# Kernel tuning notes

Measured on AMD Instinct MI355X. Metric: run time of the kernel, lower is better.

## Reference

```python
import jax, jax.numpy as jnp
import numpy as np
import math

D_MODEL = 1024
HEAD_DIM = 64
B, T = 4, 4096


def setup_inputs() -> dict:
    key = jax.random.key(0)
    kx, kq, kk, kv = jax.random.split(key, 4)
    s = 1.0 / math.sqrt(D_MODEL)  # torch Linear default init scale (approx, uniform->normal ok for ref)
    return {
        "x": jax.random.normal(kx, (B, T, D_MODEL), dtype=jnp.float32),
        "Wq": jax.random.normal(kq, (HEAD_DIM, D_MODEL), dtype=jnp.float32) * s,
        "Wk": jax.random.normal(kk, (HEAD_DIM, D_MODEL), dtype=jnp.float32) * s,
        "Wv": jax.random.normal(kv, (HEAD_DIM, D_MODEL), dtype=jnp.float32) * s,
        "energy": jnp.asarray(1.0, dtype=jnp.float32),
    }


def reference(x, Wq, Wk, Wv, energy):
    # Projections: nn.Linear(d_model, head_dim, bias=False) -> x @ W.T
    q = jnp.einsum("btc,hc->bth", x, Wq)  # [B,T,H]
    k = jnp.einsum("btc,hc->bth", x, Wk)
    v = jnp.einsum("btc,hc->bth", x, Wv)

    scale = 1.0 / math.sqrt(HEAD_DIM)
    scores = jnp.einsum("bqh,bkh->bqk", q, k) * scale  # [B,T,T]
    attn = jax.nn.softmax(scores, axis=-1)
    out = jnp.einsum("bqk,bkh->bqh", attn, v)  # [B,T,H]

    # Entropy of attention rows, averaged over batch and queries
    attn_entropy = -jnp.sum(attn * jnp.log(attn + 1e-8), axis=-1).mean()
    # Metabolic EMA side-effect (stateful in torch; returned here for completeness)
    new_energy = 0.9 * energy + 0.1 * attn_entropy

    return out, attn, new_energy
```

## Files before the change

### kernel.cpp

```cpp
#include <hip/hip_runtime.h>

#define PITCH 72

typedef __attribute__((ext_vector_type(8))) short bf16x8;
typedef __attribute__((ext_vector_type(4))) float f32x4;
typedef __attribute__((ext_vector_type(8))) unsigned short u16x8;

__device__ __forceinline__ unsigned short f2bf(float f) {
  union { float f; unsigned int u; } v; v.f = f;
  unsigned int u = v.u + 0x7fffu + ((v.u >> 16) & 1u);
  return (unsigned short)(u >> 16);
}

__device__ __forceinline__ f32x4 mfma16(bf16x8 a, bf16x8 b, f32x4 c) {
  return __builtin_amdgcn_mfma_f32_16x16x32_bf16(a, b, c, 0, 0, 0);
}

__global__ __launch_bounds__(256) void qkv_kernel(
    const float* __restrict__ x, const float* __restrict__ Wq,
    const float* __restrict__ Wk, const float* __restrict__ Wv,
    unsigned short* __restrict__ q_ws, unsigned short* __restrict__ k_ws,
    unsigned short* __restrict__ vT_ws) {
  __shared__ unsigned short Xs[64 * PITCH];
  __shared__ unsigned short Ws[192 * PITCH];

  const int tid = threadIdx.x;
  const int wave = tid >> 6, lane = tid & 63;
  const int quad = lane >> 4, l16 = lane & 15;
  const int m0 = blockIdx.x * 64;

  f32x4 acc[12];
#pragma unroll
  for (int i = 0; i < 12; ++i) acc[i] = (f32x4)0.0f;

  for (int k0 = 0; k0 < 1024; k0 += 64) {
#pragma unroll
    for (int i = 0; i < 4; ++i) {
      int cc = tid + i * 256;
      int row = cc >> 4, c4 = cc & 15;
      float4 f = *(const float4*)(x + (size_t)(m0 + row) * 1024 + k0 + c4 * 4);
      unsigned short h0 = f2bf(f.x), h1 = f2bf(f.y), h2 = f2bf(f.z), h3 = f2bf(f.w);
      ushort4 h = make_ushort4(h0, h1, h2, h3);
      *(ushort4*)&Xs[row * PITCH + c4 * 4] = h;
    }
#pragma unroll
    for (int i = 0; i < 12; ++i) {
      int cc = tid + i * 256;
      int row = cc >> 4, c4 = cc & 15;
      int which = row >> 6, wrow = row & 63;
      const float* wp = (which == 0) ? Wq : ((which == 1) ? Wk : Wv);
      float4 f = *(const float4*)(wp + (size_t)wrow * 1024 + k0 + c4 * 4);
      ushort4 h = make_ushort4(f2bf(f.x), f2bf(f.y), f2bf(f.z), f2bf(f.w));
      *(ushort4*)&Ws[row * PITCH + c4 * 4] = h;
    }
    __syncthreads();
#pragma unroll
    for (int ks = 0; ks < 64; ks += 32) {
      bf16x8 a = *(const bf16x8*)&Xs[(wave * 16 + l16) * PITCH + ks + quad * 8];
#pragma unroll
      for (int nt = 0; nt < 12; ++nt) {
        bf16x8 b = *(const bf16x8*)&Ws[(nt * 16 + l16) * PITCH + ks + quad * 8];
        acc[nt] = mfma16(a, b, acc[nt]);
      }
    }
    __syncthreads();
  }

  const int mrow = wave * 16 + quad * 4;
#pragma unroll
  for (int nt = 0; nt < 4; ++nt)
#pragma unroll
    for (int r = 0; r < 4; ++r) {
      int m = m0 + mrow + r;
      int h = nt * 16 + l16;
      q_ws[(size_t)m * 64 + h] = f2bf(acc[nt][r] * 0.125f);
    }
#pragma unroll
  for (int nt = 0; nt < 4; ++nt)
#pragma unroll
    for (int r = 0; r < 4; ++r) {
      int m = m0 + mrow + r;
      int h = nt * 16 + l16;
      k_ws[(size_t)m * 64 + h] = f2bf(acc[nt + 4][r]);
    }
  __syncthreads();
#pragma unroll
  for (int nt = 0; nt < 4; ++nt)
#pragma unroll
    for (int r = 0; r < 4; ++r)
      Xs[(nt * 16 + l16) * PITCH + mrow + r] = f2bf(acc[nt + 8][r]);
  __syncthreads();
  const int b = m0 >> 12, t0 = m0 & 4095;
#pragma unroll
  for (int i = 0; i < 2; ++i) {
    int cc = tid + i * 256;
    int h = cc >> 3, c8 = cc & 7;
    u16x8 v = *(const u16x8*)&Xs[h * PITCH + c8 * 8];
    *(u16x8*)(vT_ws + ((size_t)b * 64 + h) * 4096 + t0 + c8 * 8) = v;
  }
}

__global__ __launch_bounds__(256) void attn_kernel(
    const unsigned short* __restrict__ q_ws, const unsigned short* __restrict__ k_ws,
    const unsigned short* __restrict__ vT_ws, float* __restrict__ out,
    float* __restrict__ attn, float* __restrict__ entAcc) {
  __shared__ unsigned short Qs[64 * PITCH];
  __shared__ unsigned short Ks[64 * PITCH];
  __shared__ unsigned short Vts[64 * PITCH];
  __shared__ unsigned short Ps[4][16 * PITCH];
  __shared__ float rowS[64], rowW[64], invS[64];

  const int tid = threadIdx.x;
  const int wave = tid >> 6, lane = tid & 63;
  const int quad = lane >> 4, l16 = lane & 15;
  const int bx = blockIdx.x;
  const int b = bx >> 6, q0 = (bx & 63) * 64;

  const unsigned short* qb = q_ws + ((size_t)b * 4096 + q0) * 64;
  const unsigned short* kb = k_ws + (size_t)b * 4096 * 64;
  const unsigned short* vtb = vT_ws + (size_t)b * 64 * 4096;

#pragma unroll
  for (int i = 0; i < 2; ++i) {
    int cc = tid + i * 256;
    int row = cc >> 3, c8 = cc & 7;
    *(u16x8*)&Qs[row * PITCH + c8 * 8] = *(const u16x8*)(qb + (size_t)row * 64 + c8 * 8);
  }

  f32x4 Oacc[4];
#pragma unroll
  for (int i = 0; i < 4; ++i) Oacc[i] = (f32x4)0.0f;
  float sumE[4] = {0.f, 0.f, 0.f, 0.f};
  float sumES[4] = {0.f, 0.f, 0.f, 0.f};

  __syncthreads();

  for (int kt = 0; kt < 64; ++kt) {
    const int k0 = kt * 64;
#pragma unroll
    for (int i = 0; i < 2; ++i) {
      int cc = tid + i * 256;
      int row = cc >> 3, c8 = cc & 7;
      *(u16x8*)&Ks[row * PITCH + c8 * 8] =
          *(const u16x8*)(kb + (size_t)(k0 + row) * 64 + c8 * 8);
      *(u16x8*)&Vts[row * PITCH + c8 * 8] =
          *(const u16x8*)(vtb + (size_t)row * 4096 + k0 + c8 * 8);
    }
    __syncthreads();

    f32x4 s[4];
#pragma unroll
    for (int i = 0; i < 4; ++i) s[i] = (f32x4)0.0f;
#pragma unroll
    for (int ks = 0; ks < 64; ks += 32) {
      bf16x8 a = *(const bf16x8*)&Qs[(wave * 16 + l16) * PITCH + ks + quad * 8];
#pragma unroll
      for (int nt = 0; nt < 4; ++nt) {
        bf16x8 bk = *(const bf16x8*)&Ks[(nt * 16 + l16) * PITCH + ks + quad * 8];
        s[nt] = mfma16(a, bk, s[nt]);
      }
    }
#pragma unroll
    for (int nt = 0; nt < 4; ++nt)
#pragma unroll
      for (int r = 0; r < 4; ++r) {
        float sv = s[nt][r];
        float e = __expf(sv);
        sumE[r] += e;
        sumES[r] += e * sv;
        Ps[wave][(quad * 4 + r) * PITCH + nt * 16 + l16] = f2bf(e);
      }
#pragma unroll
    for (int kk = 0; kk < 64; kk += 32) {
      bf16x8 a = *(const bf16x8*)&Ps[wave][l16 * PITCH + kk + quad * 8];
#pragma unroll
      for (int ht = 0; ht < 4; ++ht) {
        bf16x8 bv = *(const bf16x8*)&Vts[(ht * 16 + l16) * PITCH + kk + quad * 8];
        Oacc[ht] = mfma16(a, bv, Oacc[ht]);
      }
    }
    __syncthreads();
  }

#pragma unroll
  for (int off = 1; off < 16; off <<= 1)
#pragma unroll
    for (int r = 0; r < 4; ++r) {
      sumE[r] += __shfl_xor(sumE[r], off, 64);
      sumES[r] += __shfl_xor(sumES[r], off, 64);
    }
  if (l16 == 0)
#pragma unroll
    for (int r = 0; r < 4; ++r) {
      rowS[wave * 16 + quad * 4 + r] = sumE[r];
      rowW[wave * 16 + quad * 4 + r] = sumES[r];
    }
  __syncthreads();
  if (tid < 64) {
    float S = rowS[tid], W = rowW[tid];
    float inv = 1.0f / S;
    invS[tid] = inv;
    float ent = __logf(S) - W * inv;
#pragma unroll
    for (int off = 1; off < 64; off <<= 1) ent += __shfl_xor(ent, off, 64);
    if (tid == 0) atomicAdd(entAcc, ent);
  }
  __syncthreads();

  float invR[4];
#pragma unroll
  for (int r = 0; r < 4; ++r) invR[r] = invS[wave * 16 + quad * 4 + r];

#pragma unroll
  for (int ht = 0; ht < 4; ++ht)
#pragma unroll
    for (int r = 0; r < 4; ++r) {
      int m = q0 + wave * 16 + quad * 4 + r;
      out[((size_t)b * 4096 + m) * 64 + ht * 16 + l16] = Oacc[ht][r] * invR[r];
    }

  float* attnb = attn + (size_t)b * 4096 * 4096;
  for (int kt = 0; kt < 64; ++kt) {
    const int k0 = kt * 64;
    __syncthreads();
#pragma unroll
    for (int i = 0; i < 2; ++i) {
      int cc = tid + i * 256;
      int row = cc >> 3, c8 = cc & 7;
      *(u16x8*)&Ks[row * PITCH + c8 * 8] =
          *(const u16x8*)(kb + (size_t)(k0 + row) * 64 + c8 * 8);
    }
    __syncthreads();

    f32x4 s[4];
#pragma unroll
    for (int i = 0; i < 4; ++i) s[i] = (f32x4)0.0f;
#pragma unroll
    for (int ks = 0; ks < 64; ks += 32) {
      bf16x8 a = *(const bf16x8*)&Qs[(wave * 16 + l16) * PITCH + ks + quad * 8];
#pragma unroll
      for (int nt = 0; nt < 4; ++nt) {
        bf16x8 bk = *(const bf16x8*)&Ks[(nt * 16 + l16) * PITCH + ks + quad * 8];
        s[nt] = mfma16(a, bk, s[nt]);
      }
    }
#pragma unroll
    for (int nt = 0; nt < 4; ++nt)
#pragma unroll
      for (int r = 0; r < 4; ++r) {
        float p = __expf(s[nt][r]) * invR[r];
        attnb[(size_t)(q0 + wave * 16 + quad * 4 + r) * 4096 + k0 + nt * 16 + l16] = p;
      }
  }
}

__global__ void energy_kernel(const float* __restrict__ energy,
                              const float* __restrict__ entAcc,
                              float* __restrict__ dst) {
  if (threadIdx.x == 0 && blockIdx.x == 0)
    dst[0] = 0.9f * energy[0] + 0.1f * (entAcc[0] * (1.0f / 16384.0f));
}

extern "C" void kernel_launch(void* const* d_in, const int* in_sizes, int n_in,
                              void* d_out, int out_size, void* d_ws, size_t ws_size,
                              hipStream_t stream) {
  (void)in_sizes; (void)n_in; (void)out_size; (void)ws_size;
  const float* x = (const float*)d_in[0];
  const float* Wq = (const float*)d_in[1];
  const float* Wk = (const float*)d_in[2];
  const float* Wv = (const float*)d_in[3];
  const float* energy = (const float*)d_in[4];

  float* out = (float*)d_out;
  float* attn = out + (size_t)4 * 4096 * 64;
  float* dst_energy = attn + (size_t)4 * 4096 * 4096;

  char* ws = (char*)d_ws;
  float* entAcc = (float*)ws;
  unsigned short* q_ws = (unsigned short*)(ws + 256);
  unsigned short* k_ws = q_ws + (size_t)16384 * 64;
  unsigned short* vT_ws = k_ws + (size_t)16384 * 64;

  hipMemsetAsync(entAcc, 0, sizeof(float), stream);
  qkv_kernel<<<256, 256, 0, stream>>>(x, Wq, Wk, Wv, q_ws, k_ws, vT_ws);
  attn_kernel<<<256, 256, 0, stream>>>(q_ws, k_ws, vT_ws, out, attn, entAcc);
  energy_kernel<<<1, 64, 0, stream>>>(energy, entAcc, dst_energy);
}
```

Measured before the change: 528.6 us.

## Split attention into split-K flash pass, combine, and parallel attn-matrix writer

The QKV projection now runs one block per (row tile, projection), giving 768 blocks instead of 256. The fused attention kernel is split into three kernels. A flash pass splits the key range four ways and writes partial outputs and row sums. A combine kernel reduces those partials, normalizes the output and computes entropy. A separate 8192-block kernel recomputes the scores and writes the normalized attention matrix. The aim is to fix low occupancy, since the old design had only 256 blocks each looping over all keys twice, and to spread the large attn store across many blocks. In exchange it adds workspace round-trips for the partials and extra kernel launches, and the QKV split reloads x three times.

```diff
diff --git a/kernel.cpp b/kernel.cpp
--- a/kernel.cpp
+++ b/kernel.cpp
@@ -1,6 +1,7 @@
 #include <hip/hip_runtime.h>
 
 #define PITCH 72
+#define PPITCH 68
 
 typedef __attribute__((ext_vector_type(8))) short bf16x8;
 typedef __attribute__((ext_vector_type(4))) float f32x4;
@@ -22,99 +23,91 @@
     unsigned short* __restrict__ q_ws, unsigned short* __restrict__ k_ws,
     unsigned short* __restrict__ vT_ws) {
   __shared__ unsigned short Xs[64 * PITCH];
-  __shared__ unsigned short Ws[192 * PITCH];
-
-  const int tid = threadIdx.x;
-  const int wave = tid >> 6, lane = tid & 63;
-  const int quad = lane >> 4, l16 = lane & 15;
-  const int m0 = blockIdx.x * 64;
-
-  f32x4 acc[12];
-#pragma unroll
-  for (int i = 0; i < 12; ++i) acc[i] = (f32x4)0.0f;
-
-  for (int k0 = 0; k0 < 1024; k0 += 64) {
-#pragma unroll
-    for (int i = 0; i < 4; ++i) {
-      int cc = tid + i * 256;
-      int row = cc >> 4, c4 = cc & 15;
-      float4 f = *(const float4*)(x + (size_t)(m0 + row) * 1024 + k0 + c4 * 4);
-      unsigned short h0 = f2bf(f.x), h1 = f2bf(f.y), h2 = f2bf(f.z), h3 = f2bf(f.w);
-      ushort4 h = make_ushort4(h0, h1, h2, h3);
-      *(ushort4*)&Xs[row * PITCH + c4 * 4] = h;
-    }
-#pragma unroll
-    for (int i = 0; i < 12; ++i) {
-      int cc = tid + i * 256;
-      int row = cc >> 4, c4 = cc & 15;
-      int which = row >> 6, wrow = row & 63;
-      const float* wp = (which == 0) ? Wq : ((which == 1) ? Wk : Wv);
-      float4 f = *(const float4*)(wp + (size_t)wrow * 1024 + k0 + c4 * 4);
-      ushort4 h = make_ushort4(f2bf(f.x), f2bf(f.y), f2bf(f.z), f2bf(f.w));
-      *(ushort4*)&Ws[row * PITCH + c4 * 4] = h;
-    }
-    __syncthreads();
-#pragma unroll
-    for (int ks = 0; ks < 64; ks += 32) {
-      bf16x8 a = *(const bf16x8*)&Xs[(wave * 16 + l16) * PITCH + ks + quad * 8];
-#pragma unroll
-      for (int nt = 0; nt < 12; ++nt) {
-        bf16x8 b = *(const bf16x8*)&Ws[(nt * 16 + l16) * PITCH + ks + quad * 8];
-        acc[nt] = mfma16(a, b, acc[nt]);
-      }
-    }
-    __syncthreads();
-  }
-
-  const int mrow = wave * 16 + quad * 4;
-#pragma unroll
-  for (int nt = 0; nt < 4; ++nt)
-#pragma unroll
-    for (int r = 0; r < 4; ++r) {
-      int m = m0 + mrow + r;
-      int h = nt * 16 + l16;
-      q_ws[(size_t)m * 64 + h] = f2bf(acc[nt][r] * 0.125f);
-    }
-#pragma unroll
-  for (int nt = 0; nt < 4; ++nt)
-#pragma unroll
-    for (int r = 0; r < 4; ++r) {
-      int m = m0 + mrow + r;
-      int h = nt * 16 + l16;
-      k_ws[(size_t)m * 64 + h] = f2bf(acc[nt + 4][r]);
-    }
-  __syncthreads();
-#pragma unroll
-  for (int nt = 0; nt < 4; ++nt)
-#pragma unroll
-    for (int r = 0; r < 4; ++r)
-      Xs[(nt * 16 + l16) * PITCH + mrow + r] = f2bf(acc[nt + 8][r]);
-  __syncthreads();
-  const int b = m0 >> 12, t0 = m0 & 4095;
-#pragma unroll
-  for (int i = 0; i < 2; ++i) {
-    int cc = tid + i * 256;
-    int h = cc >> 3, c8 = cc & 7;
-    u16x8 v = *(const u16x8*)&Xs[h * PITCH + c8 * 8];
-    *(u16x8*)(vT_ws + ((size_t)b * 64 + h) * 4096 + t0 + c8 * 8) = v;
-  }
-}
-
-__global__ __launch_bounds__(256) void attn_kernel(
-    const unsigned short* __restrict__ q_ws, const unsigned short* __restrict__ k_ws,
-    const unsigned short* __restrict__ vT_ws, float* __restrict__ out,
-    float* __restrict__ attn, float* __restrict__ entAcc) {
-  __shared__ unsigned short Qs[64 * PITCH];
-  __shared__ unsigned short Ks[64 * PITCH];
-  __shared__ unsigned short Vts[64 * PITCH];
-  __shared__ unsigned short Ps[4][16 * PITCH];
-  __shared__ float rowS[64], rowW[64], invS[64];
+  __shared__ unsigned short Ws[64 * PITCH];
 
   const int tid = threadIdx.x;
   const int wave = tid >> 6, lane = tid & 63;
   const int quad = lane >> 4, l16 = lane & 15;
   const int bx = blockIdx.x;
-  const int b = bx >> 6, q0 = (bx & 63) * 64;
+  const int mt = bx / 3, which = bx - mt * 3;
+  const int m0 = mt * 64;
+  const float* wp = (which == 0) ? Wq : ((which == 1) ? Wk : Wv);
+
+  f32x4 acc[4];
+#pragma unroll
+  for (int i = 0; i < 4; ++i) acc[i] = (f32x4)0.0f;
+
+  const int srow = tid >> 4, sc4 = tid & 15;
+  for (int k0 = 0; k0 < 1024; k0 += 64) {
+#pragma unroll
+    for (int i = 0; i < 4; ++i) {
+      int row = srow + i * 16;
+      float4 f = *(const float4*)(x + (size_t)(m0 + row) * 1024 + k0 + sc4 * 4);
+      *(ushort4*)&Xs[row * PITCH + sc4 * 4] =
+          make_ushort4(f2bf(f.x), f2bf(f.y), f2bf(f.z), f2bf(f.w));
+      float4 g = *(const float4*)(wp + (size_t)row * 1024 + k0 + sc4 * 4);
+      *(ushort4*)&Ws[row * PITCH + sc4 * 4] =
+          make_ushort4(f2bf(g.x), f2bf(g.y), f2bf(g.z), f2bf(g.w));
+    }
+    __syncthreads();
+#pragma unroll
+    for (int ks = 0; ks < 64; ks += 32) {
+      bf16x8 a = *(const bf16x8*)&Xs[(wave * 16 + l16) * PITCH + ks + quad * 8];
+#pragma unroll
+      for (int nt = 0; nt < 4; ++nt) {
+        bf16x8 b = *(const bf16x8*)&Ws[(nt * 16 + l16) * PITCH + ks + quad * 8];
+        acc[nt] = mfma16(a, b, acc[nt]);
+      }
+    }
+    __syncthreads();
+  }
+
+  const int mrow = wave * 16 + quad * 4;
+  if (which == 0) {
+#pragma unroll
+    for (int nt = 0; nt < 4; ++nt)
+#pragma unroll
+      for (int r = 0; r < 4; ++r)
+        q_ws[(size_t)(m0 + mrow + r) * 64 + nt * 16 + l16] = f2bf(acc[nt][r] * 0.125f);
+  } else if (which == 1) {
+#pragma unroll
+    for (int nt = 0; nt < 4; ++nt)
+#pragma unroll
+      for (int r = 0; r < 4; ++r)
+        k_ws[(size_t)(m0 + mrow + r) * 64 + nt * 16 + l16] = f2bf(acc[nt][r]);
+  } else {
+#pragma unroll
+    for (int nt = 0; nt < 4; ++nt)
+#pragma unroll
+      for (int r = 0; r < 4; ++r)
+        Xs[(nt * 16 + l16) * PITCH + mrow + r] = f2bf(acc[nt + 0][r]);
+    __syncthreads();
+    const int b = m0 >> 12, t0 = m0 & 4095;
+#pragma unroll
+    for (int i = 0; i < 2; ++i) {
+      int cc = tid + i * 256;
+      int h = cc >> 3, c8 = cc & 7;
+      u16x8 v = *(const u16x8*)&Xs[h * PITCH + c8 * 8];
+      *(u16x8*)(vT_ws + ((size_t)b * 64 + h) * 4096 + t0 + c8 * 8) = v;
+    }
+  }
+}
+
+__global__ __launch_bounds__(256) void flash_kernel(
+    const unsigned short* __restrict__ q_ws, const unsigned short* __restrict__ k_ws,
+    const unsigned short* __restrict__ vT_ws, float* __restrict__ Opart,
+    float* __restrict__ Spart, float* __restrict__ Wpart) {
+  __shared__ unsigned short Qs[64 * PITCH];
+  __shared__ unsigned short Ks[64 * PITCH];
+  __shared__ unsigned short Vts[64 * PITCH];
+  __shared__ unsigned short Ps[4][16 * PPITCH];
+
+  const int tid = threadIdx.x;
+  const int wave = tid >> 6, lane = tid & 63;
+  const int quad = lane >> 4, l16 = lane & 15;
+  const int bx = blockIdx.x;
+  const int ksp = bx & 3, qt = (bx >> 2) & 63, b = bx >> 8;
+  const int q0 = qt * 64;
 
   const unsigned short* qb = q_ws + ((size_t)b * 4096 + q0) * 64;
   const unsigned short* kb = k_ws + (size_t)b * 4096 * 64;
@@ -135,7 +128,7 @@
 
   __syncthreads();
 
-  for (int kt = 0; kt < 64; ++kt) {
+  for (int kt = ksp * 16; kt < ksp * 16 + 16; ++kt) {
     const int k0 = kt * 64;
 #pragma unroll
     for (int i = 0; i < 2; ++i) {
@@ -168,11 +161,11 @@
         float e = __expf(sv);
         sumE[r] += e;
         sumES[r] += e * sv;
-        Ps[wave][(quad * 4 + r) * PITCH + nt * 16 + l16] = f2bf(e);
+        Ps[wave][(quad * 4 + r) * PPITCH + nt * 16 + l16] = f2bf(e);
       }
 #pragma unroll
     for (int kk = 0; kk < 64; kk += 32) {
-      bf16x8 a = *(const bf16x8*)&Ps[wave][l16 * PITCH + kk + quad * 8];
+      bf16x8 a = *(const bf16x8*)&Ps[wave][l16 * PPITCH + kk + quad * 8];
 #pragma unroll
       for (int ht = 0; ht < 4; ++ht) {
         bf16x8 bv = *(const bf16x8*)&Vts[(ht * 16 + l16) * PITCH + kk + quad * 8];
@@ -189,17 +182,39 @@
       sumE[r] += __shfl_xor(sumE[r], off, 64);
       sumES[r] += __shfl_xor(sumES[r], off, 64);
     }
+  const int mrow = wave * 16 + quad * 4;
   if (l16 == 0)
 #pragma unroll
     for (int r = 0; r < 4; ++r) {
-      rowS[wave * 16 + quad * 4 + r] = sumE[r];
-      rowW[wave * 16 + quad * 4 + r] = sumES[r];
-    }
-  __syncthreads();
+      Spart[(size_t)bx * 64 + mrow + r] = sumE[r];
+      Wpart[(size_t)bx * 64 + mrow + r] = sumES[r];
+    }
+  float* Op = Opart + (size_t)bx * 4096;
+#pragma unroll
+  for (int ht = 0; ht < 4; ++ht)
+#pragma unroll
+    for (int r = 0; r < 4; ++r)
+      Op[(size_t)(mrow + r) * 64 + ht * 16 + l16] = Oacc[ht][r];
+}
+
+__global__ __launch_bounds__(256) void combine_kernel(
+    const float* __restrict__ Opart, const float* __restrict__ Spart,
+    const float* __restrict__ Wpart, float* __restrict__ out,
+    float* __restrict__ invS, float* __restrict__ entAcc) {
+  __shared__ float invLds[64];
+  const int tid = threadIdx.x;
+  const int bx = blockIdx.x;
+
   if (tid < 64) {
-    float S = rowS[tid], W = rowW[tid];
+    float S = 0.f, W = 0.f;
+#pragma unroll
+    for (int ks = 0; ks < 4; ++ks) {
+      S += Spart[(size_t)(bx * 4 + ks) * 64 + tid];
+      W += Wpart[(size_t)(bx * 4 + ks) * 64 + tid];
+    }
     float inv = 1.0f / S;
-    invS[tid] = inv;
+    invS[(size_t)bx * 64 + tid] = inv;
+    invLds[tid] = inv;
     float ent = __logf(S) - W * inv;
 #pragma unroll
     for (int off = 1; off < 64; off <<= 1) ent += __shfl_xor(ent, off, 64);
@@ -207,51 +222,77 @@
   }
   __syncthreads();
 
+  const int r = tid >> 2, cg = tid & 3;
+  float inv = invLds[r];
+#pragma unroll
+  for (int j = 0; j < 4; ++j) {
+    int c = cg * 16 + j * 4;
+    f32x4 s = (f32x4)0.0f;
+#pragma unroll
+    for (int ks = 0; ks < 4; ++ks)
+      s += *(const f32x4*)(Opart + (size_t)(bx * 4 + ks) * 4096 + r * 64 + c);
+    s *= inv;
+    *(f32x4*)(out + ((size_t)bx * 64 + r) * 64 + c) = s;
+  }
+}
+
+__global__ __launch_bounds__(256) void attn_write_kernel(
+    const unsigned short* __restrict__ q_ws, const unsigned short* __restrict__ k_ws,
+    const float* __restrict__ invS, float* __restrict__ attn) {
+  __shared__ unsigned short Qs[64 * PITCH];
+  __shared__ unsigned short Ks[128 * PITCH];
+  __shared__ float invLds[64];
+
+  const int tid = threadIdx.x;
+  const int wave = tid >> 6, lane = tid & 63;
+  const int quad = lane >> 4, l16 = lane & 15;
+  const int bx = blockIdx.x;
+  const int kc = bx & 31, qt = (bx >> 5) & 63, b = bx >> 11;
+  const int q0 = qt * 64, k0g = kc * 128;
+
+  const unsigned short* qb = q_ws + ((size_t)b * 4096 + q0) * 64;
+  const unsigned short* kb = k_ws + ((size_t)b * 4096 + k0g) * 64;
+
+#pragma unroll
+  for (int i = 0; i < 2; ++i) {
+    int cc = tid + i * 256;
+    int row = cc >> 3, c8 = cc & 7;
+    *(u16x8*)&Qs[row * PITCH + c8 * 8] = *(const u16x8*)(qb + (size_t)row * 64 + c8 * 8);
+  }
+#pragma unroll
+  for (int i = 0; i < 4; ++i) {
+    int cc = tid + i * 256;
+    int row = cc >> 3, c8 = cc & 7;
+    *(u16x8*)&Ks[row * PITCH + c8 * 8] = *(const u16x8*)(kb + (size_t)row * 64 + c8 * 8);
+  }
+  if (tid < 64) invLds[tid] = invS[(size_t)(b * 64 + qt) * 64 + tid];
+  __syncthreads();
+
+  f32x4 s[8];
+#pragma unroll
+  for (int i = 0; i < 8; ++i) s[i] = (f32x4)0.0f;
+#pragma unroll
+  for (int ks = 0; ks < 64; ks += 32) {
+    bf16x8 a = *(const bf16x8*)&Qs[(wave * 16 + l16) * PITCH + ks + quad * 8];
+#pragma unroll
+    for (int nt = 0; nt < 8; ++nt) {
+      bf16x8 bk = *(const bf16x8*)&Ks[(nt * 16 + l16) * PITCH + ks + quad * 8];
+      s[nt] = mfma16(a, bk, s[nt]);
+    }
+  }
+
   float invR[4];
 #pragma unroll
-  for (int r = 0; r < 4; ++r) invR[r] = invS[wave * 16 + quad * 4 + r];
-
-#pragma unroll
-  for (int ht = 0; ht < 4; ++ht)
+  for (int r = 0; r < 4; ++r) invR[r] = invLds[wave * 16 + quad * 4 + r];
+
+  float* ab = attn + (size_t)b * 4096 * 4096;
+#pragma unroll
+  for (int nt = 0; nt < 8; ++nt)
 #pragma unroll
     for (int r = 0; r < 4; ++r) {
       int m = q0 + wave * 16 + quad * 4 + r;
-      out[((size_t)b * 4096 + m) * 64 + ht * 16 + l16] = Oacc[ht][r] * invR[r];
-    }
-
-  float* attnb = attn + (size_t)b * 4096 * 4096;
-  for (int kt = 0; kt < 64; ++kt) {
-    const int k0 = kt * 64;
-    __syncthreads();
-#pragma unroll
-    for (int i = 0; i < 2; ++i) {
-      int cc = tid + i * 256;
-      int row = cc >> 3, c8 = cc & 7;
-      *(u16x8*)&Ks[row * PITCH + c8 * 8] =
-          *(const u16x8*)(kb + (size_t)(k0 + row) * 64 + c8 * 8);
-    }
-    __syncthreads();
-
-    f32x4 s[4];
-#pragma unroll
-    for (int i = 0; i < 4; ++i) s[i] = (f32x4)0.0f;
-#pragma unroll
-    for (int ks = 0; ks < 64; ks += 32) {
-      bf16x8 a = *(const bf16x8*)&Qs[(wave * 16 + l16) * PITCH + ks + quad * 8];
-#pragma unroll
-      for (int nt = 0; nt < 4; ++nt) {
-        bf16x8 bk = *(const bf16x8*)&Ks[(nt * 16 + l16) * PITCH + ks + quad * 8];
-        s[nt] = mfma16(a, bk, s[nt]);
-      }
-    }
-#pragma unroll
-    for (int nt = 0; nt < 4; ++nt)
-#pragma unroll
-      for (int r = 0; r < 4; ++r) {
-        float p = __expf(s[nt][r]) * invR[r];
-        attnb[(size_t)(q0 + wave * 16 + quad * 4 + r) * 4096 + k0 + nt * 16 + l16] = p;
-      }
-  }
+      ab[(size_t)m * 4096 + k0g + nt * 16 + l16] = __expf(s[nt][r]) * invR[r];
+    }
 }
 
 __global__ void energy_kernel(const float* __restrict__ energy,
@@ -280,9 +321,15 @@
   unsigned short* q_ws = (unsigned short*)(ws + 256);
   unsigned short* k_ws = q_ws + (size_t)16384 * 64;
   unsigned short* vT_ws = k_ws + (size_t)16384 * 64;
+  float* invS = (float*)(vT_ws + (size_t)16384 * 64);
+  float* Spart = invS + 16384;
+  float* Wpart = Spart + 1024 * 64;
+  float* Opart = Wpart + 1024 * 64;
 
   hipMemsetAsync(entAcc, 0, sizeof(float), stream);
-  qkv_kernel<<<256, 256, 0, stream>>>(x, Wq, Wk, Wv, q_ws, k_ws, vT_ws);
-  attn_kernel<<<256, 256, 0, stream>>>(q_ws, k_ws, vT_ws, out, attn, entAcc);
+  qkv_kernel<<<768, 256, 0, stream>>>(x, Wq, Wk, Wv, q_ws, k_ws, vT_ws);
+  flash_kernel<<<1024, 256, 0, stream>>>(q_ws, k_ws, vT_ws, Opart, Spart, Wpart);
+  combine_kernel<<<256, 256, 0, stream>>>(Opart, Spart, Wpart, out, invS, entAcc);
+  attn_write_kernel<<<8192, 256, 0, stream>>>(q_ws, k_ws, invS, attn);
   energy_kernel<<<1, 64, 0, stream>>>(energy, entAcc, dst_energy);
 }
```

Result: faster. 440.6 us (-16.6%).
